# Kernel tuning notes

Measured on AMD Instinct MI355X. Metric: run time of the kernel, lower is better.

## Reference

```python
import jax, jax.numpy as jnp
import numpy as np

B, N, E = 4, 2048, 512
H = 8
HD = E // H
HIDDEN = 3 * E  # split_ratio=3
EPS = 1e-5


def _layernorm(x, g, b):
    mu = jnp.mean(x, axis=-1, keepdims=True)
    var = jnp.var(x, axis=-1, keepdims=True)
    return (x - mu) * jax.lax.rsqrt(var + EPS) * g + b


def setup_inputs() -> dict:
    key = jax.random.key(0)
    ks = jax.random.split(key, 7)
    s = 0.02
    return {
        "x": jax.random.normal(ks[0], (B, N, E), jnp.float32),
        "qkv_w": jax.random.normal(ks[1], (E, 3 * E), jnp.float32) * s,
        "qkv_b": jax.random.normal(ks[2], (3 * E,), jnp.float32) * s,
        "fc1_w": jax.random.normal(ks[3], (E, HIDDEN), jnp.float32) * s,
        "fc1_b": jax.random.normal(ks[4], (HIDDEN,), jnp.float32) * s,
        "fc2_w": jax.random.normal(ks[5], (HIDDEN, E), jnp.float32) * s,
        "fc2_b": jax.random.normal(ks[6], (E,), jnp.float32) * s,
        "ln_att_g": jnp.ones((E,), jnp.float32),
        "ln_att_b": jnp.zeros((E,), jnp.float32),
        "ln_ffn_g": jnp.ones((E,), jnp.float32),
        "ln_ffn_b": jnp.zeros((E,), jnp.float32),
    }


def reference(x, qkv_w, qkv_b, fc1_w, fc1_b, fc2_w, fc2_b,
              ln_att_g, ln_att_b, ln_ffn_g, ln_ffn_b):
    # --- attention sub-block (pre-norm) ---
    h = x
    xn = _layernorm(x, ln_att_g, ln_att_b)
    qkv = xn @ qkv_w + qkv_b                     # [B,N,3E]
    qkv = qkv.reshape(B, N, H, 3 * HD).transpose(0, 2, 1, 3)  # [B,H,N,3*HD]
    q, k, v = jnp.split(qkv, 3, axis=-1)         # each [B,H,N,HD]
    scale = HD ** -0.5
    scores = jnp.einsum("bhnd,bhmd->bhnm", q, k) * scale
    attn = jax.nn.softmax(scores, axis=-1)
    out = jnp.einsum("bhnm,bhmd->bhnd", attn, v)
    out = out.transpose(0, 2, 1, 3).reshape(B, N, E)
    x = out + h
    # --- FFN sub-block (pre-norm) ---
    h = x
    xn = _layernorm(x, ln_ffn_g, ln_ffn_b)
    y = jax.nn.gelu(xn @ fc1_w + fc1_b, approximate=False)
    y = y @ fc2_w + fc2_b
    return y + h
```

## Files before the change

kernel.cpp:

```cpp
#include <hip/hip_runtime.h>
#include <hip/hip_bf16.h>
#include <math.h>

typedef unsigned short ushort_t;
typedef unsigned int   uint32;

typedef __bf16 bf16x8 __attribute__((ext_vector_type(8)));
typedef float  floatx4 __attribute__((ext_vector_type(4)));

__device__ __forceinline__ float lo16(uint32 u) { return __uint_as_float(u << 16); }
__device__ __forceinline__ float hi16(uint32 u) { return __uint_as_float(u & 0xFFFF0000u); }
__device__ __forceinline__ float b2f(ushort_t u) { return __uint_as_float(((uint32)u) << 16); }
__device__ __forceinline__ ushort_t f2b(float f) {
    uint32 x = __float_as_uint(f);
    x += 0x7FFFu + ((x >> 16) & 1u);
    return (ushort_t)(x >> 16);
}
__device__ __forceinline__ bool bf_mode(const uint32* sniff) {
    return *sniff == 0x3F803F80u;
}
__device__ __forceinline__ float rd(const void* p, size_t i, bool bf) {
    return bf ? b2f(((const ushort_t*)p)[i]) : ((const float*)p)[i];
}
__device__ __forceinline__ float4 rd4(const void* p, size_t i, bool bf) {
    if (bf) {
        uint2 u = *(const uint2*)((const ushort_t*)p + i);
        float4 r; r.x = lo16(u.x); r.y = hi16(u.x); r.z = lo16(u.y); r.w = hi16(u.y);
        return r;
    }
    return *(const float4*)((const float*)p + i);
}
__device__ __forceinline__ float fexp2(float x) {
#if __has_builtin(__builtin_amdgcn_exp2f)
    return __builtin_amdgcn_exp2f(x);
#else
    return exp2f(x);
#endif
}
__device__ __forceinline__ uint32 pack_bf16(float e0, float e1) {
#if __has_builtin(__builtin_amdgcn_perm)
    return __builtin_amdgcn_perm(__float_as_uint(e1), __float_as_uint(e0), 0x07060302u);
#else
    return (__float_as_uint(e0) >> 16) | (__float_as_uint(e1) & 0xFFFF0000u);
#endif
}
__device__ __forceinline__ void async_cp16(const ushort_t* g, ushort_t* l) {
    __builtin_amdgcn_global_load_lds(
        (const __attribute__((address_space(1))) void*)g,
        (__attribute__((address_space(3))) void*)l, 16, 0, 0);
}
__device__ __forceinline__ float gelu_f(float x) {
    float u = 0.79788456f * x * (1.0f + 0.044715f * x * x);
    u = fminf(u, 40.0f);
    float e = exp2f(u * 2.88539008f);
    return x * e * __builtin_amdgcn_rcpf(e + 1.0f);
}

__global__ __launch_bounds__(256)
void sentinel(float* out, float val, int n)
{
    int i = blockIdx.x * 256 + threadIdx.x;
    if (i < n) out[i] = val;
}

__global__ __launch_bounds__(256)
void fuse_pre(const void* __restrict__ w0, const void* __restrict__ w1,
              const void* __restrict__ w2, ushort_t* __restrict__ t0,
              ushort_t* __restrict__ t1, ushort_t* __restrict__ t2,
              const void* __restrict__ x, const void* __restrict__ g,
              const void* __restrict__ bta, ushort_t* __restrict__ xout,
              const uint32* __restrict__ sniff)
{
    __shared__ ushort_t s[32][33];
    bool bf = bf_mode(sniff);
    int bx = blockIdx.x;
    if (bx < 2304) {
        int z = bx / 768, b768 = bx % 768;
        const void* W  = (z == 0) ? w0 : (z == 1) ? w1 : w2;
        ushort_t* Wt   = (z == 0) ? t0 : (z == 1) ? t1 : t2;
        int K = (z == 2) ? 1536 : 512;
        int N = (z == 2) ? 512 : 1536;
        int nb = N >> 5;
        int n0 = (b768 % nb) * 32, k0 = (b768 / nb) * 32;
        int tx = threadIdx.x & 31, ty = threadIdx.x >> 5;
#pragma unroll
        for (int i = 0; i < 4; i++) {
            int r = ty + i * 8;
            s[r][tx] = f2b(rd(W, (size_t)(k0 + r) * N + (n0 + tx), bf));
        }
        __syncthreads();
#pragma unroll
        for (int i = 0; i < 4; i++) {
            int r = ty + i * 8;
            Wt[(size_t)(n0 + r) * K + (k0 + tx)] = s[tx][r];
        }
    } else {
        int wid = threadIdx.x >> 6, lane = threadIdx.x & 63;
        int row = (bx - 2304) * 4 + wid;
        size_t base = (size_t)row * 512 + (size_t)lane * 8;
        float4 v0 = rd4(x, base, bf), v1 = rd4(x, base + 4, bf);
        float v[8] = {v0.x, v0.y, v0.z, v0.w, v1.x, v1.y, v1.z, v1.w};
        float sm = 0.f, ss = 0.f;
#pragma unroll
        for (int i = 0; i < 8; i++) { sm += v[i]; ss += v[i] * v[i]; }
#pragma unroll
        for (int off = 32; off; off >>= 1) {
            sm += __shfl_xor(sm, off);
            ss += __shfl_xor(ss, off);
        }
        float mu  = sm * (1.0f / 512.0f);
        float var = ss * (1.0f / 512.0f) - mu * mu;
        float rs  = rsqrtf(var + 1e-5f);
        float4 g0 = rd4(g, lane * 8, bf), g1 = rd4(g, lane * 8 + 4, bf);
        float4 b0 = rd4(bta, lane * 8, bf), b1 = rd4(bta, lane * 8 + 4, bf);
        float gv[8] = {g0.x, g0.y, g0.z, g0.w, g1.x, g1.y, g1.z, g1.w};
        float bv[8] = {b0.x, b0.y, b0.z, b0.w, b1.x, b1.y, b1.z, b1.w};
        ushort_t o[8];
#pragma unroll
        for (int i = 0; i < 8; i++) o[i] = f2b((v[i] - mu) * rs * gv[i] + bv[i]);
        uint4 ov;
        ov.x = (uint32)o[0] | ((uint32)o[1] << 16);
        ov.y = (uint32)o[2] | ((uint32)o[3] << 16);
        ov.z = (uint32)o[4] | ((uint32)o[5] << 16);
        ov.w = (uint32)o[6] | ((uint32)o[7] << 16);
        *(uint4*)(xout + base) = ov;
    }
}

__global__ __launch_bounds__(256)
void v_transpose(const ushort_t* __restrict__ hbuf, ushort_t* __restrict__ vt)
{
    __shared__ ushort_t s[32][33];
    int tx = threadIdx.x & 31, ty = threadIdx.x >> 5;
    int n0 = blockIdx.x * 32, d0 = blockIdx.y * 32;
    int bh = blockIdx.z;
    int b = bh >> 3, h = bh & 7;
#pragma unroll
    for (int i = 0; i < 4; i++) {
        int r = ty + i * 8;
        s[r][tx] = hbuf[(size_t)(b * 2048 + n0 + r) * 1536 + h * 192 + 128 + d0 + tx];
    }
    __syncthreads();
    int pt = ((tx & 12) << 1) | ((tx & 16) >> 2) | (tx & 3);
#pragma unroll
    for (int i = 0; i < 4; i++) {
        int r = ty + i * 8;
        vt[((size_t)bh * 64 + d0 + r) * 2048 + n0 + pt] = s[tx][r];
    }
}

template <int XMODE>
__global__ __launch_bounds__(256)
void ln_any(const void* __restrict__ x, const void* __restrict__ g,
            const void* __restrict__ bta, ushort_t* __restrict__ out,
            const uint32* __restrict__ sniff)
{
    bool bf = bf_mode(sniff);
    int wid = threadIdx.x >> 6, lane = threadIdx.x & 63;
    int row = blockIdx.x * 4 + wid;
    size_t base = (size_t)row * 512 + (size_t)lane * 8;

    float4 v0, v1;
    if (XMODE == 2) { v0 = rd4(x, base, false); v1 = rd4(x, base + 4, false); }
    else            { v0 = rd4(x, base, bf);    v1 = rd4(x, base + 4, bf); }
    float v[8] = {v0.x, v0.y, v0.z, v0.w, v1.x, v1.y, v1.z, v1.w};

    float s = 0.f, ss = 0.f;
#pragma unroll
    for (int i = 0; i < 8; i++) { s += v[i]; ss += v[i] * v[i]; }
#pragma unroll
    for (int off = 32; off; off >>= 1) {
        s  += __shfl_xor(s, off);
        ss += __shfl_xor(ss, off);
    }
    float mu  = s * (1.0f / 512.0f);
    float var = ss * (1.0f / 512.0f) - mu * mu;
    float rs  = rsqrtf(var + 1e-5f);

    float4 g0 = rd4(g, lane * 8, bf), g1 = rd4(g, lane * 8 + 4, bf);
    float4 b0 = rd4(bta, lane * 8, bf), b1 = rd4(bta, lane * 8 + 4, bf);
    float gv[8] = {g0.x, g0.y, g0.z, g0.w, g1.x, g1.y, g1.z, g1.w};
    float bv[8] = {b0.x, b0.y, b0.z, b0.w, b1.x, b1.y, b1.z, b1.w};

    ushort_t o[8];
#pragma unroll
    for (int i = 0; i < 8; i++) o[i] = f2b((v[i] - mu) * rs * gv[i] + bv[i]);
    uint4 ov;
    ov.x = (uint32)o[0] | ((uint32)o[1] << 16);
    ov.y = (uint32)o[2] | ((uint32)o[3] << 16);
    ov.z = (uint32)o[4] | ((uint32)o[5] << 16);
    ov.w = (uint32)o[6] | ((uint32)o[7] << 16);
    *(uint4*)(out + base) = ov;
}

template <int TI, int TJ, int MODE>
__global__ __launch_bounds__(512)
void gemm_bt(const ushort_t* __restrict__ A, const ushort_t* __restrict__ Bt,
             const void* __restrict__ bias, void* C,
             const float* resid, ushort_t* __restrict__ vtw,
             int M, int N, int K, const uint32* __restrict__ sniff)
{
    constexpr int BM = 64 * TI;
    constexpr int BN = 32 * TJ;
    constexpr bool SW = (MODE == 1 || MODE == 2);
    __shared__ ushort_t As[2][BM][32];
    __shared__ ushort_t Bs[2][BN][32];

    bool bf = bf_mode(sniff);
    int tid = threadIdx.x;
    int wid = tid >> 6, lane = tid & 63;

    int nwgx = gridDim.x;
    int wg   = blockIdx.y * nwgx + blockIdx.x;
    int cpx  = (nwgx * gridDim.y) >> 3;
    int swz  = (wg & 7) * cpx + (wg >> 3);
    int m0 = (swz / nwgx) * BM, n0 = (swz % nwgx) * BN;

    int wm = (wid >> 1) * (16 * TI), wn = (wid & 1) * (16 * TJ);
    int lm = lane & 15, kq = lane >> 4;

    floatx4 acc[TI][TJ];
#pragma unroll
    for (int i = 0; i < TI; i++)
#pragma unroll
        for (int j = 0; j < TJ; j++) acc[i][j] = (floatx4)(0.f);

    auto stage = [&](int k0, int q) {
#pragma unroll
        for (int i = 0; i < (BM * 64) / 8192; i++) {
            int lin = i * 512 + tid;
            int r = lin >> 2, c8 = (lin & 3) * 8;
            async_cp16(&A[(size_t)(m0 + r) * K + k0 + c8], &As[q][r][c8]);
        }
        if constexpr ((BN * 64) >= 8192) {
#pragma unroll
            for (int i = 0; i < (BN * 64) / 8192; i++) {
                int lin = i * 512 + tid;
                int r = lin >> 2, c8 = (lin & 3) * 8;
                async_cp16(&Bt[(size_t)(n0 + r) * K + k0 + c8], &Bs[q][r][c8]);
            }
        } else {
            if (tid < BN * 4) {
                int r = tid >> 2, c8 = (tid & 3) * 8;
                async_cp16(&Bt[(size_t)(n0 + r) * K + k0 + c8], &Bs[q][r][c8]);
            }
        }
    };

    stage(0, 0);
    stage(32, 1);
    __syncthreads();

    int p = 0;
    for (int k0 = 0; k0 < K; k0 += 32) {
        bf16x8 af[TI], bfr[TJ];
#pragma unroll
        for (int ti = 0; ti < TI; ti++)
            af[ti] = *(const bf16x8*)&As[p][wm + ti * 16 + lm][kq * 8];
#pragma unroll
        for (int tj = 0; tj < TJ; tj++)
            bfr[tj] = *(const bf16x8*)&Bs[p][wn + tj * 16 + lm][kq * 8];

        __syncthreads();
        if (k0 + 64 < K) stage(k0 + 64, p);

#pragma unroll
        for (int ti = 0; ti < TI; ti++)
#pragma unroll
            for (int tj = 0; tj < TJ; tj++) {
                if (SW)
                    acc[ti][tj] = __builtin_amdgcn_mfma_f32_16x16x32_bf16(
                        bfr[tj], af[ti], acc[ti][tj], 0, 0, 0);
                else
                    acc[ti][tj] = __builtin_amdgcn_mfma_f32_16x16x32_bf16(
                        af[ti], bfr[tj], acc[ti][tj], 0, 0, 0);
            }
        p ^= 1;
    }

    if (SW) {
#pragma unroll
        for (int ti = 0; ti < TI; ti++) {
            int row = m0 + wm + ti * 16 + lm;
#pragma unroll
            for (int tj = 0; tj < TJ; tj++) {
                int cb = n0 + wn + tj * 16 + kq * 4;
                float4 b4 = rd4(bias, cb, bf);
                float v0 = acc[ti][tj][0] + b4.x;
                float v1 = acc[ti][tj][1] + b4.y;
                float v2 = acc[ti][tj][2] + b4.z;
                float v3 = acc[ti][tj][3] + b4.w;
                if (MODE == 1) {
                    v0 = gelu_f(v0); v1 = gelu_f(v1);
                    v2 = gelu_f(v2); v3 = gelu_f(v3);
                    uint2 ov;
                    ov.x = (uint32)f2b(v0) | ((uint32)f2b(v1) << 16);
                    ov.y = (uint32)f2b(v2) | ((uint32)f2b(v3) << 16);
                    *(uint2*)((ushort_t*)C + (size_t)row * N + cb) = ov;
                } else {
                    float4 rv = *(const float4*)&resid[(size_t)row * N + cb];
                    float4 ov;
                    ov.x = v0 + rv.x; ov.y = v1 + rv.y;
                    ov.z = v2 + rv.z; ov.w = v3 + rv.w;
                    *(float4*)((float*)C + (size_t)row * N + cb) = ov;
                }
            }
        }
    } else {
        float bv[TJ];
#pragma unroll
        for (int tj = 0; tj < TJ; tj++) bv[tj] = rd(bias, n0 + wn + tj * 16 + lm, bf);
#pragma unroll
        for (int ti = 0; ti < TI; ti++) {
            int grow_base = m0 + wm + ti * 16 + kq * 4;
#pragma unroll
            for (int tj = 0; tj < TJ; tj++) {
                int gcol = n0 + wn + tj * 16 + lm;
                if (MODE == 3 && (gcol % 192) >= 128) {
                    int h2 = gcol / 192, d = (gcol % 192) - 128;
                    int bq = grow_base >> 11, nloc = grow_base & 2047;
                    int posb = (nloc & ~31) | ((nloc & 12) << 1) | ((nloc & 16) >> 2);
                    uint2 ov;
                    ov.x = (uint32)f2b(acc[ti][tj][0] + bv[tj]) |
                           ((uint32)f2b(acc[ti][tj][1] + bv[tj]) << 16);
                    ov.y = (uint32)f2b(acc[ti][tj][2] + bv[tj]) |
                           ((uint32)f2b(acc[ti][tj][3] + bv[tj]) << 16);
                    *(uint2*)&vtw[((size_t)(bq * 8 + h2) * 64 + d) * 2048 + posb] = ov;
                } else {
#pragma unroll
                    for (int r = 0; r < 4; r++) {
                        int grow = grow_base + r;
                        float v = acc[ti][tj][r] + bv[tj];
                        ((ushort_t*)C)[(size_t)grow * N + gcol] = f2b(v);
                    }
                }
            }
        }
    }
}

template <int MODE>
__global__ __launch_bounds__(256)
void vgemm(const ushort_t* __restrict__ A, const void* __restrict__ W,
           const void* __restrict__ bias, void* C,
           const float* resid, int M, int N, int K,
             const uint32* __restrict__ sniff)
{
    __shared__ float Ast[32][33];
    __shared__ float Bs[32][36];

    bool bf = bf_mode(sniff);
    int t  = threadIdx.x;
    int tx = t & 15, ty = t >> 4;
    int m0 = blockIdx.y * 32, n0 = blockIdx.x * 32;
    int sr = t >> 3, sc4 = (t & 7) * 4;

    float a00 = 0.f, a01 = 0.f, a10 = 0.f, a11 = 0.f;

    for (int k0 = 0; k0 < K; k0 += 32) {
        __syncthreads();
        {
            uint2 u = *(const uint2*)&A[(size_t)(m0 + sr) * K + k0 + sc4];
            Ast[sc4 + 0][sr] = lo16(u.x);
            Ast[sc4 + 1][sr] = hi16(u.x);
            Ast[sc4 + 2][sr] = lo16(u.y);
            Ast[sc4 + 3][sr] = hi16(u.y);
        }
        {
            float4 w = rd4(W, (size_t)(k0 + sr) * N + n0 + sc4, bf);
            *(float4*)&Bs[sr][sc4] = w;
        }
        __syncthreads();

#pragma unroll
        for (int kk = 0; kk < 32; kk++) {
            float av0 = Ast[kk][ty], av1 = Ast[kk][ty + 16];
            float bv0 = Bs[kk][tx],  bv1 = Bs[kk][tx + 16];
            a00 += av0 * bv0; a01 += av0 * bv1;
            a10 += av1 * bv0; a11 += av1 * bv1;
        }
    }

    float accs[4] = {a00, a01, a10, a11};
#pragma unroll
    for (int q = 0; q < 4; q++) {
        int row = m0 + ty + (q >> 1) * 16;
        int col = n0 + tx + (q & 1) * 16;
        float v = accs[q] + rd(bias, col, bf);
        if (MODE == 1) v = gelu_f(v);
        if (MODE == 2) {
            float rv = resid[(size_t)row * N + col];
            ((float*)C)[(size_t)row * N + col] = v + rv;
        } else {
            ((ushort_t*)C)[(size_t)row * N + col] = f2b(v);
        }
    }
}

__global__ __launch_bounds__(512)
void attn_flash(const ushort_t* __restrict__ qkv, const ushort_t* __restrict__ vt,
                const void* __restrict__ x, float* __restrict__ out,
                const uint32* __restrict__ sniff)
{
    __shared__ ushort_t Kl[2][2][64][72];
    __shared__ ushort_t Vl[2][2][64][72];

    bool bf = bf_mode(sniff);
    int tid = threadIdx.x;
    int wid = tid >> 6;
    int wlocal = wid & 3;
    int grp = wid >> 2;
    int lane = tid & 63;
    int lm = lane & 15, quad = lane >> 4;

    int bid = blockIdx.x;
    int swz = (bid & 7) * 64 + (bid >> 3);
    int qt = swz & 15;
    int h  = (swz >> 4) & 7;
    int b  = swz >> 7;
    int bh = b * 8 + h;
    int q0 = qt * 128;

    const float SC = 0.18033688011f;

    bf16x8 qf[2][2];
#pragma unroll
    for (int g = 0; g < 2; g++) {
        const ushort_t* qp = qkv +
            ((size_t)(b * 2048 + q0 + wlocal * 32 + g * 16 + lm) * 1536 + h * 192);
        union { bf16x8 v; ushort_t u[8]; } qa0, qa1;
        qa0.v = *(const bf16x8*)(qp + quad * 8);
        qa1.v = *(const bf16x8*)(qp + 32 + quad * 8);
#pragma unroll
        for (int i = 0; i < 8; i++) {
            qa0.u[i] = f2b(b2f(qa0.u[i]) * SC);
            qa1.u[i] = f2b(b2f(qa1.u[i]) * SC);
        }
        qf[g][0] = qa0.v; qf[g][1] = qa1.v;
    }

    floatx4 oacc[2][4];
#pragma unroll
    for (int g = 0; g < 2; g++)
#pragma unroll
        for (int dt = 0; dt < 4; dt++) oacc[g][dt] = (floatx4)(0.f);
    float lsum[2] = {0.f, 0.f};

    int t256 = tid & 255;
    int srow = t256 >> 3;
    int sc8  = (t256 & 7) * 8;
    int kv0  = grp * 1024;

    const ushort_t* kb0 = qkv + ((size_t)(b * 2048 + kv0 + srow) * 1536 + h * 192 + 64 + sc8);
    const ushort_t* kb1 = qkv + ((size_t)(b * 2048 + kv0 + 32 + srow) * 1536 + h * 192 + 64 + sc8);
    const ushort_t* vb0 = vt + ((size_t)(bh * 64 + srow) * 2048 + kv0 + sc8);
    const ushort_t* vb1 = vt + ((size_t)(bh * 64 + 32 + srow) * 2048 + kv0 + sc8);

    uint4 kr0 = *(const uint4*)(kb0);
    uint4 kr1 = *(const uint4*)(kb1);
    uint4 vr0 = *(const uint4*)(vb0);
    uint4 vr1 = *(const uint4*)(vb1);
    *(uint4*)&Kl[grp][0][srow][sc8]      = kr0;
    *(uint4*)&Kl[grp][0][32 + srow][sc8] = kr1;
    *(uint4*)&Vl[grp][0][srow][sc8]      = vr0;
    *(uint4*)&Vl[grp][0][32 + srow][sc8] = vr1;
    kr0 = *(const uint4*)(kb0 + (size_t)64 * 1536);
    kr1 = *(const uint4*)(kb1 + (size_t)64 * 1536);
    vr0 = *(const uint4*)(vb0 + 64);
    vr1 = *(const uint4*)(vb1 + 64);
    __syncthreads();

    int p = 0;
    for (int kvl = 0; kvl < 1024; kvl += 64) {
        if (kvl < 1024 - 64) {
            *(uint4*)&Kl[grp][p ^ 1][srow][sc8]      = kr0;
            *(uint4*)&Kl[grp][p ^ 1][32 + srow][sc8] = kr1;
            *(uint4*)&Vl[grp][p ^ 1][srow][sc8]      = vr0;
            *(uint4*)&Vl[grp][p ^ 1][32 + srow][sc8] = vr1;
            int nkv = (kvl + 128) & 1023;
            kr0 = *(const uint4*)(kb0 + (size_t)nkv * 1536);
            kr1 = *(const uint4*)(kb1 + (size_t)nkv * 1536);
            vr0 = *(const uint4*)(vb0 + nkv);
            vr1 = *(const uint4*)(vb1 + nkv);
        }

        floatx4 sacc[2][4];
#pragma unroll
        for (int g = 0; g < 2; g++)
#pragma unroll
            for (int t = 0; t < 4; t++) sacc[g][t] = (floatx4)(0.f);
        __builtin_amdgcn_s_setprio(1);
#pragma unroll
        for (int t = 0; t < 4; t++) {
            bf16x8 kf0 = *(const bf16x8*)&Kl[grp][p][t * 16 + lm][quad * 8];
            bf16x8 kf1 = *(const bf16x8*)&Kl[grp][p][t * 16 + lm][32 + quad * 8];
#pragma unroll
            for (int g = 0; g < 2; g++) {
                sacc[g][t] = __builtin_amdgcn_mfma_f32_16x16x32_bf16(kf0, qf[g][0], sacc[g][t], 0, 0, 0);
                sacc[g][t] = __builtin_amdgcn_mfma_f32_16x16x32_bf16(kf1, qf[g][1], sacc[g][t], 0, 0, 0);
            }
        }
        __builtin_amdgcn_s_setprio(0);

        uint32 pk[2][4][2];
#pragma unroll
        for (int g = 0; g < 2; g++)
#pragma unroll
            for (int t = 0; t < 4; t++) {
                float e0 = fexp2(sacc[g][t][0]);
                float e1 = fexp2(sacc[g][t][1]);
                float e2 = fexp2(sacc[g][t][2]);
                float e3 = fexp2(sacc[g][t][3]);
                lsum[g] += (e0 + e1) + (e2 + e3);
                pk[g][t][0] = pack_bf16(e0, e1);
                pk[g][t][1] = pack_bf16(e2, e3);
            }

        __builtin_amdgcn_s_setprio(1);
#pragma unroll
        for (int dt = 0; dt < 4; dt++) {
            bf16x8 vf0 = *(const bf16x8*)&Vl[grp][p][dt * 16 + lm][quad * 8];
            bf16x8 vf1 = *(const bf16x8*)&Vl[grp][p][dt * 16 + lm][32 + quad * 8];
#pragma unroll
            for (int g = 0; g < 2; g++) {
                union { uint4 u; bf16x8 v; } c0, c1;
                c0.u = make_uint4(pk[g][0][0], pk[g][0][1], pk[g][1][0], pk[g][1][1]);
                c1.u = make_uint4(pk[g][2][0], pk[g][2][1], pk[g][3][0], pk[g][3][1]);
                oacc[g][dt] = __builtin_amdgcn_mfma_f32_16x16x32_bf16(c0.v, vf0, oacc[g][dt], 0, 0, 0);
                oacc[g][dt] = __builtin_amdgcn_mfma_f32_16x16x32_bf16(c1.v, vf1, oacc[g][dt], 0, 0, 0);
            }
        }
        __builtin_amdgcn_s_setprio(0);

        __syncthreads();
        p ^= 1;
    }

    float lred[2];
#pragma unroll
    for (int g = 0; g < 2; g++) {
        float rs = lsum[g];
        rs += __shfl_xor(rs, 16);
        rs += __shfl_xor(rs, 32);
        lred[g] = rs;
    }

    float* Ofl = (float*)&Kl[0][0][0][0];
    float* Lfl = Ofl + 128 * 68;
    if (grp == 1) {
#pragma unroll
        for (int g = 0; g < 2; g++) {
#pragma unroll
            for (int dt = 0; dt < 4; dt++)
#pragma unroll
                for (int r = 0; r < 4; r++)
                    Ofl[(wlocal * 32 + g * 16 + quad * 4 + r) * 68 + dt * 16 + lm]
                        = oacc[g][dt][r];
            if (quad == 0) Lfl[wlocal * 32 + g * 16 + lm] = lred[g];
        }
    }
    __syncthreads();
    if (grp == 0) {
        float rinv[2][4];
#pragma unroll
        for (int g = 0; g < 2; g++) {
            float rt = lred[g] + Lfl[wlocal * 32 + g * 16 + lm];
            float ri = __builtin_amdgcn_rcpf(rt);
#pragma unroll
            for (int r = 0; r < 4; r++)
                rinv[g][r] = __shfl(ri, quad * 4 + r);
        }
#pragma unroll
        for (int g = 0; g < 2; g++)
#pragma unroll
            for (int dt = 0; dt < 4; dt++)
#pragma unroll
                for (int r = 0; r < 4; r++) {
                    int rl = wlocal * 32 + g * 16 + quad * 4 + r;
                    float o = oacc[g][dt][r] + Ofl[rl * 68 + dt * 16 + lm];
                    int row = q0 + rl;
                    int col = h * 64 + dt * 16 + lm;
                    size_t idx = (size_t)(b * 2048 + row) * 512 + col;
                    out[idx] = o * rinv[g][r] + rd(x, idx, bf);
                }
    }
}

extern "C" void kernel_launch(void* const* d_in, const int* in_sizes, int n_in,
                              void* d_out, int out_size, void* d_ws, size_t ws_size,
                              hipStream_t stream)
{
    static const int expect[11] = {4194304, 786432, 1536, 786432, 1536, 786432,
                                   512, 512, 512, 512, 512};
    bool ok = (n_in == 11);
    if (ok) for (int i = 0; i < 11; i++) if (in_sizes[i] != expect[i]) { ok = false; break; }
    int nblk = (out_size + 255) / 256;
    if (!ok) {
        sentinel<<<nblk, 256, 0, stream>>>((float*)d_out, 1.0e6f, out_size);
        return;
    }
    if (ws_size < (size_t)33554432) {
        sentinel<<<nblk, 256, 0, stream>>>((float*)d_out, 2.0e6f, out_size);
        return;
    }

    const void* x     = d_in[0];
    const void* qkv_w = d_in[1];
    const void* qkv_b = d_in[2];
    const void* fc1_w = d_in[3];
    const void* fc1_b = d_in[4];
    const void* fc2_w = d_in[5];
    const void* fc2_b = d_in[6];
    const void* ln1g  = d_in[7];
    const void* ln1b  = d_in[8];
    const void* ln2g  = d_in[9];
    const void* ln2b  = d_in[10];
    const uint32* sniff = (const uint32*)d_in[7];

    char* ws = (char*)d_ws;
    ushort_t* xn   = (ushort_t*)(ws);
    ushort_t* hbuf = (ushort_t*)(ws + 8388608);
    float*    x2   = (float*)d_out;

    bool mfma_path = (ws_size >= (size_t)38273024);
    bool vt_own    = (ws_size >= (size_t)46661632);

    if (mfma_path) {
        ushort_t* wtq = (ushort_t*)(ws + 33554432);
        ushort_t* wt1 = (ushort_t*)(ws + 35127296);
        ushort_t* wt2 = (ushort_t*)(ws + 36700160);
        ushort_t* vt  = vt_own ? (ushort_t*)(ws + 38273024) : xn;

        fuse_pre<<<4352, 256, 0, stream>>>(qkv_w, fc1_w, fc2_w, wtq, wt1, wt2,
                                           x, ln1g, ln1b, xn, sniff);
        if (vt_own) {
            gemm_bt<2, 4, 3><<<dim3(12, 64), 512, 0, stream>>>(
                xn, wtq, qkv_b, hbuf, nullptr, vt, 8192, 1536, 512, sniff);
        } else {
            gemm_bt<2, 4, 0><<<dim3(12, 64), 512, 0, stream>>>(
                xn, wtq, qkv_b, hbuf, nullptr, nullptr, 8192, 1536, 512, sniff);
            v_transpose<<<dim3(64, 2, 32), 256, 0, stream>>>(hbuf, vt);
        }
        attn_flash<<<512, 512, 0, stream>>>(hbuf, vt, x, x2, sniff);
        ln_any<2><<<2048, 256, 0, stream>>>(x2, ln2g, ln2b, xn, sniff);
        gemm_bt<2, 4, 1><<<dim3(12, 64), 512, 0, stream>>>(
            xn, wt1, fc1_b, hbuf, nullptr, nullptr, 8192, 1536, 512, sniff);
        gemm_bt<2, 2, 2><<<dim3(8, 64), 512, 0, stream>>>(
            hbuf, wt2, fc2_b, d_out, x2, nullptr, 8192, 512, 1536, sniff);
    } else {
        ushort_t* vt = xn;
        ln_any<0><<<2048, 256, 0, stream>>>(x, ln1g, ln1b, xn, sniff);
        vgemm<0><<<dim3(48, 256), 256, 0, stream>>>(xn, qkv_w, qkv_b, hbuf, nullptr,
                                                    8192, 1536, 512, sniff);
        v_transpose<<<dim3(64, 2, 32), 256, 0, stream>>>(hbuf, vt);
        attn_flash<<<512, 512, 0, stream>>>(hbuf, vt, x, x2, sniff);
        ln_any<2><<<2048, 256, 0, stream>>>(x2, ln2g, ln2b, xn, sniff);
        vgemm<1><<<dim3(48, 256), 256, 0, stream>>>(xn, fc1_w, fc1_b, hbuf, nullptr,
                                                    8192, 1536, 512, sniff);
        vgemm<2><<<dim3(16, 256), 256, 0, stream>>>(hbuf, fc2_w, fc2_b, d_out, x2,
                                                    8192, 512, 1536, sniff);
    }
}
```

Baseline: 219.5 us.

## Add 256x256-tile MFMA GEMM with XCD swizzle for QKV and FC1

Adds a new GEMM kernel using 256x256 output tiles with a K-step of 64, double-buffered async copies into LDS, an XCD-aware workgroup swizzle, and s_setprio around MFMA bursts. It replaces the QKV and FC1 GEMMs, which used 128x128 tiles. The aim is more data reuse per LDS load and better L2 locality across chiplets. In exchange it uses 128KB of LDS and limits occupancy to one block per CU, and the 192-block grid leaves some of the 256 CUs idle.

```diff
diff --git a/kernel.cpp b/kernel.cpp
--- a/kernel.cpp
+++ b/kernel.cpp
@@ -191,6 +191,150 @@
     ov.z = (uint32)o[4] | ((uint32)o[5] << 16);
     ov.w = (uint32)o[6] | ((uint32)o[7] << 16);
     *(uint4*)(out + base) = ov;
+}
+
+template <int MODE>
+__global__ __launch_bounds__(512, 1)
+void gemm8(const ushort_t* __restrict__ A, const ushort_t* __restrict__ Bt,
+           const void* __restrict__ bias, void* C,
+           ushort_t* __restrict__ vtw,
+           int M, int N, int K, const uint32* __restrict__ sniff)
+{
+    __shared__ ushort_t As[2][256][64];
+    __shared__ ushort_t Bs[2][256][64];
+
+    bool bf = bf_mode(sniff);
+    int tid = threadIdx.x;
+    int wid = tid >> 6, lane = tid & 63;
+
+    int nwgx = gridDim.x;
+    int wg   = blockIdx.y * nwgx + blockIdx.x;
+    int cpx  = (nwgx * gridDim.y) >> 3;
+    int swz  = (wg & 7) * cpx + (wg >> 3);
+    int m0 = (swz / nwgx) * 256, n0 = (swz % nwgx) * 256;
+
+    int wr = wid >> 2, wc = wid & 3;
+    int lm = lane & 15, kq = lane >> 4;
+
+    floatx4 acc[8][4];
+#pragma unroll
+    for (int i = 0; i < 8; i++)
+#pragma unroll
+        for (int j = 0; j < 4; j++) acc[i][j] = (floatx4)(0.f);
+
+    auto stage = [&](int t, int s) {
+        int k0 = t * 64;
+#pragma unroll
+        for (int i = 0; i < 4; i++) {
+            int lin = i * 512 + tid;
+            int r = lin >> 3, c8 = (lin & 7) * 8;
+            async_cp16(&A[(size_t)(m0 + r) * K + k0 + c8], &As[s][r][c8]);
+        }
+#pragma unroll
+        for (int i = 0; i < 4; i++) {
+            int lin = i * 512 + tid;
+            int r = lin >> 3, c8 = (lin & 7) * 8;
+            async_cp16(&Bt[(size_t)(n0 + r) * K + k0 + c8], &Bs[s][r][c8]);
+        }
+    };
+
+    int nt = K >> 6;
+
+    stage(0, 0);
+    stage(1, 1);
+    asm volatile("s_waitcnt vmcnt(8)" ::: "memory");
+    __builtin_amdgcn_s_barrier();
+    __builtin_amdgcn_sched_barrier(0);
+
+    for (int t = 0; t < nt; t++) {
+        int s = t & 1;
+#pragma unroll
+        for (int kc = 0; kc < 2; kc++) {
+            bf16x8 af[8], bfv[4];
+#pragma unroll
+            for (int mi = 0; mi < 8; mi++)
+                af[mi] = *(const bf16x8*)&As[s][wr * 128 + mi * 16 + lm][kc * 32 + kq * 8];
+#pragma unroll
+            for (int ni = 0; ni < 4; ni++)
+                bfv[ni] = *(const bf16x8*)&Bs[s][wc * 64 + ni * 16 + lm][kc * 32 + kq * 8];
+            __builtin_amdgcn_s_setprio(1);
+#pragma unroll
+            for (int mi = 0; mi < 8; mi++)
+#pragma unroll
+                for (int ni = 0; ni < 4; ni++) {
+                    if (MODE == 1)
+                        acc[mi][ni] = __builtin_amdgcn_mfma_f32_16x16x32_bf16(
+                            bfv[ni], af[mi], acc[mi][ni], 0, 0, 0);
+                    else
+                        acc[mi][ni] = __builtin_amdgcn_mfma_f32_16x16x32_bf16(
+                            af[mi], bfv[ni], acc[mi][ni], 0, 0, 0);
+                }
+            __builtin_amdgcn_s_setprio(0);
+        }
+        if (t == nt - 1) break;
+
+        __builtin_amdgcn_sched_barrier(0);
+        __builtin_amdgcn_s_barrier();
+        if (t + 2 < nt) {
+            stage(t + 2, s);
+            asm volatile("s_waitcnt vmcnt(8)" ::: "memory");
+        } else {
+            asm volatile("s_waitcnt vmcnt(0)" ::: "memory");
+        }
+        __builtin_amdgcn_s_barrier();
+        __builtin_amdgcn_sched_barrier(0);
+    }
+
+    if (MODE == 1) {
+#pragma unroll
+        for (int mi = 0; mi < 8; mi++) {
+            int row = m0 + wr * 128 + mi * 16 + lm;
+#pragma unroll
+            for (int ni = 0; ni < 4; ni++) {
+                int cb = n0 + wc * 64 + ni * 16 + kq * 4;
+                float4 b4 = rd4(bias, cb, bf);
+                float v0 = gelu_f(acc[mi][ni][0] + b4.x);
+                float v1 = gelu_f(acc[mi][ni][1] + b4.y);
+                float v2 = gelu_f(acc[mi][ni][2] + b4.z);
+                float v3 = gelu_f(acc[mi][ni][3] + b4.w);
+                uint2 ov;
+                ov.x = (uint32)f2b(v0) | ((uint32)f2b(v1) << 16);
+                ov.y = (uint32)f2b(v2) | ((uint32)f2b(v3) << 16);
+                *(uint2*)((ushort_t*)C + (size_t)row * N + cb) = ov;
+            }
+        }
+    } else {
+        float bv[4];
+#pragma unroll
+        for (int ni = 0; ni < 4; ni++)
+            bv[ni] = rd(bias, n0 + wc * 64 + ni * 16 + lm, bf);
+#pragma unroll
+        for (int mi = 0; mi < 8; mi++) {
+            int grow_base = m0 + wr * 128 + mi * 16 + kq * 4;
+#pragma unroll
+            for (int ni = 0; ni < 4; ni++) {
+                int gcol = n0 + wc * 64 + ni * 16 + lm;
+                if (MODE == 3 && (gcol % 192) >= 128) {
+                    int h2 = gcol / 192, d = (gcol % 192) - 128;
+                    int bq = grow_base >> 11, nloc = grow_base & 2047;
+                    int posb = (nloc & ~31) | ((nloc & 12) << 1) | ((nloc & 16) >> 2);
+                    uint2 ov;
+                    ov.x = (uint32)f2b(acc[mi][ni][0] + bv[ni]) |
+                           ((uint32)f2b(acc[mi][ni][1] + bv[ni]) << 16);
+                    ov.y = (uint32)f2b(acc[mi][ni][2] + bv[ni]) |
+                           ((uint32)f2b(acc[mi][ni][3] + bv[ni]) << 16);
+                    *(uint2*)&vtw[((size_t)(bq * 8 + h2) * 64 + d) * 2048 + posb] = ov;
+                } else {
+#pragma unroll
+                    for (int r = 0; r < 4; r++) {
+                        int grow = grow_base + r;
+                        float v = acc[mi][ni][r] + bv[ni];
+                        ((ushort_t*)C)[(size_t)grow * N + gcol] = f2b(v);
+                    }
+                }
+            }
+        }
+    }
 }
 
 template <int TI, int TJ, int MODE>
@@ -634,8 +778,8 @@
         fuse_pre<<<4352, 256, 0, stream>>>(qkv_w, fc1_w, fc2_w, wtq, wt1, wt2,
                                            x, ln1g, ln1b, xn, sniff);
         if (vt_own) {
-            gemm_bt<2, 4, 3><<<dim3(12, 64), 512, 0, stream>>>(
-                xn, wtq, qkv_b, hbuf, nullptr, vt, 8192, 1536, 512, sniff);
+            gemm8<3><<<dim3(6, 32), 512, 0, stream>>>(
+                xn, wtq, qkv_b, hbuf, vt, 8192, 1536, 512, sniff);
         } else {
             gemm_bt<2, 4, 0><<<dim3(12, 64), 512, 0, stream>>>(
                 xn, wtq, qkv_b, hbuf, nullptr, nullptr, 8192, 1536, 512, sniff);
@@ -643,8 +787,8 @@
         }
         attn_flash<<<512, 512, 0, stream>>>(hbuf, vt, x, x2, sniff);
         ln_any<2><<<2048, 256, 0, stream>>>(x2, ln2g, ln2b, xn, sniff);
-        gemm_bt<2, 4, 1><<<dim3(12, 64), 512, 0, stream>>>(
-            xn, wt1, fc1_b, hbuf, nullptr, nullptr, 8192, 1536, 512, sniff);
+        gemm8<1><<<dim3(6, 32), 512, 0, stream>>>(
+            xn, wt1, fc1_b, hbuf, nullptr, 8192, 1536, 512, sniff);
         gemm_bt<2, 2, 2><<<dim3(8, 64), 512, 0, stream>>>(
             hbuf, wt2, fc2_b, d_out, x2, nullptr, 8192, 512, 1536, sniff);
     } else {
```

New measurement: 237.0 us. +8.0%, slower.
